# Optimization experiments

Measured on AMD Instinct MI355X. Metric: run time of the kernel, lower is better.

Reference implementation:

```python
import jax, jax.numpy as jnp
import numpy as np

N = 1024      # num_nodes
U = 64        # num_units
IN_DIM = 2    # input feature dim per node
B = 32        # batch
F = IN_DIM + U  # 66, input_size inside _gconv


def _xavier(k, shape):
    fan_in, fan_out = shape[-2], shape[-1]
    std = (2.0 / (fan_in + fan_out)) ** 0.5
    return jax.random.normal(k, shape, jnp.float32) * std


def setup_inputs() -> dict:
    key = jax.random.key(0)
    ks = jax.random.split(key, 14)
    return {
        "inputs": jax.random.normal(ks[0], (B, N * IN_DIM), jnp.float32),
        "hx": jax.random.normal(ks[1], (B, N * U), jnp.float32),
        "adj": jax.random.uniform(ks[2], (2, N, N), jnp.float32),
        "mask": jax.random.uniform(ks[3], (8, N, N), jnp.float32),
        # gate gconv params (output_size = 2U). Note: torch LayerParams caches by
        # shape, so weights_s/weights_i/weights_bp are ONE shared weight, ditto atts/atti.
        "W_ru": _xavier(ks[4], (F, 2 * U)),
        "Watt_ru": _xavier(ks[5], (N, 2 * U, 2 * U)),
        "Watt1_ru": _xavier(ks[6], (N, 2 * U, 1)),
        "Wout_ru": _xavier(ks[7], (6 * U, 2 * U)),
        "b_ru": jnp.ones((2 * U,), jnp.float32),   # bias_start=1.0
        # candidate gconv params (output_size = U)
        "W_c": _xavier(ks[8], (F, U)),
        "Watt_c": _xavier(ks[9], (N, U, U)),
        "Watt1_c": _xavier(ks[10], (N, U, 1)),
        "Wout_c": _xavier(ks[11], (3 * U, U)),
        "b_c": jnp.zeros((U,), jnp.float32),
    }


def _gconv(inputs, state, adj, mask, W, Watt, Watt1, Wout, b):
    Bs = inputs.shape[0]
    x = jnp.concatenate([inputs.reshape(Bs, N, -1), state.reshape(Bs, N, -1)], axis=2)  # [B,N,F]
    Ff = x.shape[2]
    x0 = x.transpose(1, 2, 0).reshape(N, Ff * Bs)  # [N, F*B]
    a0, a1 = adj[0], adj[1]
    # supports in the exact order of the torch loop:
    # adj0, mask0..3*adj0, mask4..7*adj1, adj1  -> 10 matrices
    mats = jnp.concatenate(
        [a0[None], mask[:4] * a0[None], mask[4:] * a1[None], a1[None]], axis=0
    )  # [10,N,N]
    xk = jnp.einsum('mij,jf->mif', mats, x0)  # [10,N,F*B]
    x_all = jnp.concatenate([x0[None], xk], axis=0).reshape(11, N, Ff, Bs)
    x_bp = x_all[0].transpose(2, 0, 1)        # [B,N,F]
    x_i = x_all[1:6].transpose(3, 1, 0, 2)    # [B,N,5,F]
    x_s = x_all[6:].transpose(3, 1, 0, 2)     # [B,N,5,F]
    x_i_p = x_i @ W        # [B,N,5,O] (shared weight, see LayerParams shape cache)
    x_s_p = x_s @ W        # [B,N,5,O]
    x_bp_p = x_bp @ W      # [B,N,O]

    def attend(xp):
        h = jax.nn.relu(jnp.einsum('bnko,noq->bnkq', xp, Watt))     # per-node weights
        s = jnp.einsum('bnkq,nqo->bnko', h, Watt1)[..., 0]          # [B,N,5]
        a = jax.nn.softmax(s, axis=-1)                              # over 5 supports
        return jnp.einsum('bnk,bnko->bno', a, xp)                   # [B,N,O]

    xi = attend(x_i_p)
    xs = attend(x_s_p)
    out = jnp.concatenate([xi, xs, x_bp_p], axis=-1) @ Wout + b     # [B,N,O]
    return out.reshape(Bs, -1)


def reference(inputs, hx, adj, mask, W_ru, Watt_ru, Watt1_ru, Wout_ru, b_ru,
              W_c, Watt_c, Watt1_c, Wout_c, b_c):
    value = jax.nn.sigmoid(_gconv(inputs, hx, adj, mask, W_ru, Watt_ru, Watt1_ru, Wout_ru, b_ru))
    value = value.reshape(-1, N, 2 * U)
    r = value[..., :U].reshape(-1, N * U)
    u = value[..., U:].reshape(-1, N * U)
    c = jnp.tanh(_gconv(inputs, r * hx, adj, mask, W_c, Watt_c, Watt1_c, Wout_c, b_c))
    return u * hx + (1.0 - u) * c
```

## Files before the change

### kernel.cpp

```cpp
#include <hip/hip_runtime.h>
#include <hip/hip_fp16.h>
#include <cstdint>
#include <cstddef>

#define NN 1024
#define BB 32

typedef _Float16 f16x8 __attribute__((ext_vector_type(8)));
typedef _Float16 f16x4 __attribute__((ext_vector_type(4)));
typedef float f32x4 __attribute__((ext_vector_type(4)));
typedef float f32x16 __attribute__((ext_vector_type(16)));

__device__ __forceinline__ void load_lds16(const void* g, void* l) {
  __builtin_amdgcn_global_load_lds(
      (const __attribute__((address_space(1))) void*)g,
      (__attribute__((address_space(3))) void*)l, 16, 0, 0);
}

__global__ __launch_bounds__(256) void k_build_amats(
    const float* __restrict__ adj, const float* __restrict__ mask,
    _Float16* __restrict__ A) {
  int q = blockIdx.x * 256 + threadIdx.x;
  int i = q >> 8;
  int j0 = (q & 255) << 2;
  size_t off = (size_t)i * 1024 + j0;
  float4 a0 = *(const float4*)(adj + off);
  float4 a1 = *(const float4*)(adj + (1u << 20) + off);
  f16x4 r;
  r[0] = a0.x; r[1] = a0.y; r[2] = a0.z; r[3] = a0.w;
  *(f16x4*)(A + off) = r;
  r[0] = a1.x; r[1] = a1.y; r[2] = a1.z; r[3] = a1.w;
  *(f16x4*)(A + (size_t)9 * 1048576 + off) = r;
#pragma unroll
  for (int l = 0; l < 8; ++l) {
    float4 mk = *(const float4*)(mask + (size_t)l * 1048576 + off);
    float4 base = (l < 4) ? a0 : a1;
    r[0] = mk.x * base.x; r[1] = mk.y * base.y;
    r[2] = mk.z * base.z; r[3] = mk.w * base.w;
    *(f16x4*)(A + (size_t)(l + 1) * 1048576 + off) = r;
  }
}

__global__ __launch_bounds__(256) void k_prep_wout(
    const float* __restrict__ Wru, const float* __restrict__ Wc,
    _Float16* __restrict__ WThru, _Float16* __restrict__ WTlru,
    _Float16* __restrict__ WThc, _Float16* __restrict__ WTlc) {
  int id = blockIdx.x * 256 + threadIdx.x;
  if (id < 128 * 384) {
    int o = id & 127, k = id >> 7;
    float w = Wru[k * 128 + o];
    _Float16 h = (_Float16)w;
    WThru[o * 384 + k] = h;
    WTlru[o * 384 + k] = (_Float16)(w - (float)h);
  } else {
    int id2 = id - 128 * 384;
    if (id2 < 64 * 192) {
      int o = id2 & 63, k = id2 >> 6;
      float w = Wc[k * 64 + o];
      _Float16 h = (_Float16)w;
      WThc[o * 192 + k] = h;
      WTlc[o * 192 + k] = (_Float16)(w - (float)h);
    }
  }
}

__global__ __launch_bounds__(256) void k_build_x0p(
    const float* __restrict__ inp, const float* __restrict__ state,
    _Float16* __restrict__ X0P) {
  const int b = blockIdx.x;
  const int j0 = blockIdx.y * 64;
  const int tid = threadIdx.x;
  for (int p = tid; p < 4096; p += 256) {
    int jj = p >> 6, f = p & 63;
    X0P[((size_t)(b * 1024 + j0 + jj)) * 96 + 2 + f] =
        (_Float16)state[(size_t)b * 65536 + (j0 + jj) * 64 + f];
  }
  if (tid < 128) {
    int jj = tid >> 1, f = tid & 1;
    X0P[((size_t)(b * 1024 + j0 + jj)) * 96 + f] =
        (_Float16)inp[(size_t)b * 2048 + (j0 + jj) * 2 + f];
    X0P[((size_t)(b * 1024 + j0 + 32 + jj)) * 96 + f] =
        (_Float16)inp[(size_t)b * 2048 + (j0 + 32 + jj) * 2 + f];
  }
  for (int p = tid; p < 64 * 32; p += 256) {
    int jj = p >> 5, f = 66 + (p & 31);
    if (f < 96)
      X0P[((size_t)(b * 1024 + j0 + jj)) * 96 + f] = (_Float16)0.f;
  }
}

template <int O>
__global__ __launch_bounds__(256, 2) void k_proj0_mfma(
    const _Float16* __restrict__ X0P, const float* __restrict__ W,
    _Float16* __restrict__ XP0, _Float16* __restrict__ XP0T) {
  constexpr int WR = O / 64;
  constexpr int WC = 4 / WR;
  constexpr int TN = WC * 64;
  constexpr int NPT = TN / 64;
  __shared__ _Float16 ldsB[2][TN * 32];
  const int tid = threadIdx.x;
  const int c0 = blockIdx.x * TN;
  const int b = c0 >> 10;
  const int l = tid & 63;
  const int w = tid >> 6;
  const int wr = w / WC, wc = w % WC;

  f16x8 af[4][3];
#pragma unroll
  for (int i = 0; i < 4; ++i) {
    int o = wr * 64 + i * 16 + (l & 15);
#pragma unroll
    for (int ks = 0; ks < 3; ++ks) {
#pragma unroll
      for (int e = 0; e < 8; ++e) {
        int f = ks * 32 + (l >> 4) * 8 + e;
        af[i][ks][e] = (f < 66) ? (_Float16)W[f * O + o] : (_Float16)0.f;
      }
    }
  }

  int tt[NPT], rr[NPT], qq[NPT];
#pragma unroll
  for (int u = 0; u < NPT; ++u) {
    tt[u] = u * 256 + tid;
    rr[u] = tt[u] >> 2;
    qq[u] = (tt[u] & 3) ^ (rr[u] & 3);
  }

  const int ps = ((l >> 4) ^ (l & 3)) * 8;
  int offB[4];
#pragma unroll
  for (int j = 0; j < 4; ++j)
    offB[j] = (wc * 64 + j * 16 + (l & 15)) * 32 + ps;

  f32x4 acc[4][4];
#pragma unroll
  for (int i = 0; i < 4; ++i)
#pragma unroll
    for (int j = 0; j < 4; ++j) acc[i][j] = (f32x4){0.f, 0.f, 0.f, 0.f};

#pragma unroll
  for (int u = 0; u < NPT; ++u)
    load_lds16(X0P + (size_t)(c0 + rr[u]) * 96 + qq[u] * 8,
               &ldsB[0][0] + tt[u] * 8);

  int buf = 0;
  for (int kt = 0; kt < 3; ++kt) {
    __syncthreads();
    if (kt + 1 < 3) {
#pragma unroll
      for (int u = 0; u < NPT; ++u)
        load_lds16(X0P + (size_t)(c0 + rr[u]) * 96 + (kt + 1) * 32 + qq[u] * 8,
                   &ldsB[buf ^ 1][0] + tt[u] * 8);
    }
    f16x8 bf[4];
#pragma unroll
    for (int j = 0; j < 4; ++j) bf[j] = *(const f16x8*)(&ldsB[buf][offB[j]]);
#pragma unroll
    for (int i = 0; i < 4; ++i)
#pragma unroll
      for (int j = 0; j < 4; ++j)
        acc[i][j] = __builtin_amdgcn_mfma_f32_16x16x32_f16(af[i][kt], bf[j],
                                                           acc[i][j], 0, 0, 0);
    buf ^= 1;
  }

#pragma unroll
  for (int i = 0; i < 4; ++i) {
    int ob = wr * 64 + i * 16 + (l >> 4) * 4;
#pragma unroll
    for (int j = 0; j < 4; ++j) {
      int jn = (c0 & 1023) + wc * 64 + j * 16 + (l & 15);
      f16x4 hv;
#pragma unroll
      for (int r = 0; r < 4; ++r) {
        hv[r] = (_Float16)acc[i][j][r];
        XP0T[((size_t)b * O + ob + r) * 1024 + jn] = hv[r];
      }
      *(f16x4*)(XP0 + ((size_t)jn * 32 + b) * O + ob) = hv;
    }
  }
}

template <int CN>
__global__ __launch_bounds__(256, 2) void k_supports2_mfma(
    const _Float16* __restrict__ A, const _Float16* __restrict__ BT,
    _Float16* __restrict__ XPD) {
  __shared__ _Float16 ldsA[2][4096];
  __shared__ _Float16 ldsB[2][4096];
  const int tid = threadIdx.x;
  constexpr int GX = CN / 128;
  const int flat = blockIdx.x + GX * blockIdx.y;
  constexpr int NWG = GX * 80;
  constexpr int CPX = NWG / 8;
  const int swz = (flat & 7) * CPX + (flat >> 3);
  const int bn = swz % GX;
  const int bm = swz / GX;
  const int l = tid & 63;
  const int w = tid >> 6;
  const int wr = w >> 1, wc = w & 1;

  const int t0 = tid, t1 = 256 + tid;
  const int r0 = t0 >> 2, q0 = (t0 & 3) ^ (r0 & 3);
  const int r1 = t1 >> 2, q1 = (t1 & 3) ^ (r1 & 3);
  const _Float16* gA0 = A + ((size_t)(bm * 128 + r0)) * 1024 + q0 * 8;
  const _Float16* gA1 = A + ((size_t)(bm * 128 + r1)) * 1024 + q1 * 8;
  const _Float16* gB0 = BT + ((size_t)(bn * 128 + r0)) * 1024 + q0 * 8;
  const _Float16* gB1 = BT + ((size_t)(bn * 128 + r1)) * 1024 + q1 * 8;

  int offA[2][2], offB[2][2];
#pragma unroll
  for (int fi = 0; fi < 2; ++fi)
#pragma unroll
    for (int ks = 0; ks < 2; ++ks) {
      int slot = ((ks * 2 + (l >> 5)) ^ (l & 3)) * 8;
      offA[fi][ks] = (wr * 64 + fi * 32 + (l & 31)) * 32 + slot;
      offB[fi][ks] = (wc * 64 + fi * 32 + (l & 31)) * 32 + slot;
    }

  f32x16 acc[2][2];
#pragma unroll
  for (int i = 0; i < 2; ++i)
#pragma unroll
    for (int j = 0; j < 2; ++j)
#pragma unroll
      for (int e = 0; e < 16; ++e) acc[i][j][e] = 0.f;

  load_lds16(gA0, &ldsA[0][0] + t0 * 8);
  load_lds16(gA1, &ldsA[0][0] + t1 * 8);
  load_lds16(gB0, &ldsB[0][0] + t0 * 8);
  load_lds16(gB1, &ldsB[0][0] + t1 * 8);

  int buf = 0;
  for (int kt = 0; kt < 32; ++kt) {
    __syncthreads();
    if (kt + 1 < 32) {
      int k0 = (kt + 1) * 32;
      load_lds16(gA0 + k0, &ldsA[buf ^ 1][0] + t0 * 8);
      load_lds16(gA1 + k0, &ldsA[buf ^ 1][0] + t1 * 8);
      load_lds16(gB0 + k0, &ldsB[buf ^ 1][0] + t0 * 8);
      load_lds16(gB1 + k0, &ldsB[buf ^ 1][0] + t1 * 8);
    }
    f16x8 af[2][2], bf[2][2];
#pragma unroll
    for (int fi = 0; fi < 2; ++fi)
#pragma unroll
      for (int ks = 0; ks < 2; ++ks) {
        af[fi][ks] = *(const f16x8*)(&ldsA[buf][offA[fi][ks]]);
        bf[fi][ks] = *(const f16x8*)(&ldsB[buf][offB[fi][ks]]);
      }
#pragma unroll
    for (int fi = 0; fi < 2; ++fi)
#pragma unroll
      for (int fj = 0; fj < 2; ++fj)
#pragma unroll
        for (int ks = 0; ks < 2; ++ks)
          acc[fi][fj] = __builtin_amdgcn_mfma_f32_32x32x16_f16(
              af[fi][ks], bf[fj][ks], acc[fi][fj], 0, 0, 0);
    buf ^= 1;
  }

#pragma unroll
  for (int fi = 0; fi < 2; ++fi)
#pragma unroll
    for (int fj = 0; fj < 2; ++fj) {
      int colg = bn * 128 + wc * 64 + fj * 32 + (l & 31);
      int Rb = bm * 128 + wr * 64 + fi * 32 + 4 * (l >> 5);
#pragma unroll
      for (int e = 0; e < 16; ++e) {
        int R = Rb + (e & 3) + 8 * (e >> 2);
        XPD[(size_t)R * CN + colg] = (_Float16)acc[fi][fj][e];
      }
    }
}

template <int O>
__global__ __launch_bounds__(256) void k_attend_mfma(
    const __half* __restrict__ XPD, const float* __restrict__ Watt,
    const float* __restrict__ Watt1, _Float16* __restrict__ CAT2h,
    _Float16* __restrict__ CAT2l) {
  constexpr int MTW = O / 64;
  constexpr int KS = O / 32;
  constexpr int SLOTS = O / 8;
  constexpr int SWZ = SLOTS - 1;
  constexpr int OH = O / 2;
  const int n = blockIdx.x;
  const int tid = threadIdx.x;
  const int l = tid & 63;
  const int w = tid >> 6;

  __shared__ _Float16 xpL[160 * O];
  __shared__ float sPartL[4][160];
  __shared__ float aL[32][5];

  const int qbase = w * (O / 4);
  f16x8 afr[MTW][KS];
#pragma unroll
  for (int mt = 0; mt < MTW; ++mt) {
    const int q = qbase + mt * 16 + (l & 15);
#pragma unroll
    for (int ks = 0; ks < KS; ++ks) {
#pragma unroll
      for (int e = 0; e < 8; ++e) {
        int o = ks * 32 + (l >> 4) * 8 + e;
        afr[mt][ks][e] = (_Float16)Watt[((size_t)n * O + o) * O + q];
      }
    }
  }
  float wt1[MTW][4];
#pragma unroll
  for (int mt = 0; mt < MTW; ++mt)
#pragma unroll
    for (int r = 0; r < 4; ++r)
      wt1[mt][r] = Watt1[(size_t)n * O + qbase + mt * 16 + (l >> 4) * 4 + r];

  for (int g = 0; g < 2; ++g) {
    if (g) __syncthreads();
    {
      const uint32_t* xsrc = reinterpret_cast<const uint32_t*>(XPD);
      uint32_t* xdst = reinterpret_cast<uint32_t*>(xpL);
      for (int p = tid; p < 160 * OH; p += 256) {
        int row = p / OH;
        int oh = p - row * OH;
        int slot = oh >> 2;
        int phys = slot ^ (row & SWZ);
        int si = row >> 5, b = row & 31;
        size_t gi = ((size_t)(g * 5 + si) * 1024 + n) * (size_t)(16 * O) +
                    b * OH + oh;
        xdst[row * OH + phys * 4 + (oh & 3)] = xsrc[gi];
      }
    }
    __syncthreads();

    for (int nt = 0; nt < 10; ++nt) {
      f32x4 acc[MTW];
#pragma unroll
      for (int mt = 0; mt < MTW; ++mt) acc[mt] = (f32x4){0.f, 0.f, 0.f, 0.f};
      const int row = nt * 16 + (l & 15);
#pragma unroll
      for (int ks = 0; ks < KS; ++ks) {
        int phys = (ks * 4 + (l >> 4)) ^ (row & SWZ);
        f16x8 bf = *(const f16x8*)(&xpL[row * O + phys * 8]);
#pragma unroll
        for (int mt = 0; mt < MTW; ++mt)
          acc[mt] = __builtin_amdgcn_mfma_f32_16x16x32_f16(afr[mt][ks], bf,
                                                           acc[mt], 0, 0, 0);
      }
      float sp = 0.f;
#pragma unroll
      for (int mt = 0; mt < MTW; ++mt)
#pragma unroll
        for (int r = 0; r < 4; ++r)
          sp += fmaxf(acc[mt][r], 0.f) * wt1[mt][r];
      sp += __shfl_xor(sp, 16);
      sp += __shfl_xor(sp, 32);
      if (l < 16) sPartL[w][nt * 16 + l] = sp;
    }
    __syncthreads();

    if (tid < 32) {
      const int b = tid;
      float sv[5];
#pragma unroll
      for (int k = 0; k < 5; ++k) {
        int row = k * 32 + b;
        sv[k] = sPartL[0][row] + sPartL[1][row] + sPartL[2][row] +
                sPartL[3][row];
      }
      float mx = sv[0];
#pragma unroll
      for (int k = 1; k < 5; ++k) mx = fmaxf(mx, sv[k]);
      float e[5], sum = 0.f;
#pragma unroll
      for (int k = 0; k < 5; ++k) {
        e[k] = expf(sv[k] - mx);
        sum += e[k];
      }
      float inv = 1.f / sum;
#pragma unroll
      for (int k = 0; k < 5; ++k) aL[b][k] = e[k] * inv;
    }
    __syncthreads();

    for (int it = 0; it < SLOTS * 32 / 256; ++it) {
      int idx = it * 256 + tid;
      int b = idx & 31;
      int sc = idx >> 5;
      float o8[8] = {0.f, 0.f, 0.f, 0.f, 0.f, 0.f, 0.f, 0.f};
#pragma unroll
      for (int si = 0; si < 5; ++si) {
        int row = si * 32 + b;
        int phys = sc ^ (row & SWZ);
        f16x8 xv = *(const f16x8*)(&xpL[row * O + phys * 8]);
        float a = aL[b][si];
#pragma unroll
        for (int j = 0; j < 8; ++j) o8[j] += a * (float)xv[j];
      }
      f16x8 hv, lv;
#pragma unroll
      for (int j = 0; j < 8; ++j) {
        hv[j] = (_Float16)o8[j];
        lv[j] = (_Float16)(o8[j] - (float)hv[j]);
      }
      size_t doff = ((size_t)n * 32 + b) * (2 * O) + g * O + sc * 8;
      *reinterpret_cast<f16x8*>(CAT2h + doff) = hv;
      *reinterpret_cast<f16x8*>(CAT2l + doff) = lv;
    }
  }
}

__global__ __launch_bounds__(256, 2) void k_wout_ru_mfma(
    const _Float16* __restrict__ CAT2h, const _Float16* __restrict__ CAT2l,
    const _Float16* __restrict__ XP0, const _Float16* __restrict__ WTh,
    const _Float16* __restrict__ WTl, const float* __restrict__ bias,
    const float* __restrict__ hx, float* __restrict__ RHX,
    float* __restrict__ UBUF) {
  constexpr int KTOT = 384, KC = 8, KT = 12;
  __shared__ _Float16 ldsAh[2][4096];
  __shared__ _Float16 ldsAl[2][4096];
  __shared__ _Float16 ldsBh[2][4096];
  __shared__ _Float16 ldsBl[2][4096];
  const int tid = threadIdx.x;
  const int blk = blockIdx.x;
  const int l = tid & 63;
  const int w = tid >> 6;
  const int wr = w >> 1, wc = w & 1;

  const int t0 = tid, t1 = 256 + tid;
  const int r0 = t0 >> 2, q0 = (t0 & 3) ^ (r0 & 3);
  const int r1 = t1 >> 2, q1 = (t1 & 3) ^ (r1 & 3);
  const size_t R0 = (size_t)blk * 128 + r0, R1 = (size_t)blk * 128 + r1;
  const _Float16* pA0ch = CAT2h + R0 * 256 + q0 * 8;
  const _Float16* pA1ch = CAT2h + R1 * 256 + q1 * 8;
  const _Float16* pA0cl = CAT2l + R0 * 256 + q0 * 8;
  const _Float16* pA1cl = CAT2l + R1 * 256 + q1 * 8;
  const _Float16* pA0x = XP0 + R0 * 128 + q0 * 8;
  const _Float16* pA1x = XP0 + R1 * 128 + q1 * 8;
  const _Float16* pB0h = WTh + (size_t)r0 * KTOT + q0 * 8;
  const _Float16* pB1h = WTh + (size_t)r1 * KTOT + q1 * 8;
  const _Float16* pB0l = WTl + (size_t)r0 * KTOT + q0 * 8;
  const _Float16* pB1l = WTl + (size_t)r1 * KTOT + q1 * 8;

  const int ps = ((l >> 4) ^ (l & 3)) * 8;
  int offA[4], offB[4];
#pragma unroll
  for (int i = 0; i < 4; ++i) {
    offA[i] = (wr * 64 + i * 16 + (l & 15)) * 32 + ps;
    offB[i] = (wc * 64 + i * 16 + (l & 15)) * 32 + ps;
  }

  f32x4 acc[4][4];
#pragma unroll
  for (int i = 0; i < 4; ++i)
#pragma unroll
    for (int j = 0; j < 4; ++j) acc[i][j] = (f32x4){0.f, 0.f, 0.f, 0.f};

  load_lds16(pA0ch, &ldsAh[0][0] + t0 * 8);
  load_lds16(pA1ch, &ldsAh[0][0] + t1 * 8);
  load_lds16(pA0cl, &ldsAl[0][0] + t0 * 8);
  load_lds16(pA1cl, &ldsAl[0][0] + t1 * 8);
  load_lds16(pB0h, &ldsBh[0][0] + t0 * 8);
  load_lds16(pB1h, &ldsBh[0][0] + t1 * 8);
  load_lds16(pB0l, &ldsBl[0][0] + t0 * 8);
  load_lds16(pB1l, &ldsBl[0][0] + t1 * 8);

  int buf = 0;
  for (int kt = 0; kt < KT; ++kt) {
    __syncthreads();
    if (kt + 1 < KT) {
      int k1 = kt + 1;
      const _Float16* a0 =
          (k1 < KC) ? pA0ch + k1 * 32 : pA0x + (k1 - KC) * 32;
      const _Float16* a1 =
          (k1 < KC) ? pA1ch + k1 * 32 : pA1x + (k1 - KC) * 32;
      load_lds16(a0, &ldsAh[buf ^ 1][0] + t0 * 8);
      load_lds16(a1, &ldsAh[buf ^ 1][0] + t1 * 8);
      if (k1 < KC) {
        load_lds16(pA0cl + k1 * 32, &ldsAl[buf ^ 1][0] + t0 * 8);
        load_lds16(pA1cl + k1 * 32, &ldsAl[buf ^ 1][0] + t1 * 8);
      }
      load_lds16(pB0h + k1 * 32, &ldsBh[buf ^ 1][0] + t0 * 8);
      load_lds16(pB1h + k1 * 32, &ldsBh[buf ^ 1][0] + t1 * 8);
      load_lds16(pB0l + k1 * 32, &ldsBl[buf ^ 1][0] + t0 * 8);
      load_lds16(pB1l + k1 * 32, &ldsBl[buf ^ 1][0] + t1 * 8);
    }
    f16x8 ah[4], bh[4], bl[4];
#pragma unroll
    for (int i = 0; i < 4; ++i) ah[i] = *(const f16x8*)(&ldsAh[buf][offA[i]]);
#pragma unroll
    for (int i = 0; i < 4; ++i) bh[i] = *(const f16x8*)(&ldsBh[buf][offB[i]]);
#pragma unroll
    for (int i = 0; i < 4; ++i) bl[i] = *(const f16x8*)(&ldsBl[buf][offB[i]]);
#pragma unroll
    for (int i = 0; i < 4; ++i)
#pragma unroll
      for (int j = 0; j < 4; ++j) {
        acc[i][j] = __builtin_amdgcn_mfma_f32_16x16x32_f16(ah[i], bh[j],
                                                           acc[i][j], 0, 0, 0);
        acc[i][j] = __builtin_amdgcn_mfma_f32_16x16x32_f16(ah[i], bl[j],
                                                           acc[i][j], 0, 0, 0);
      }
    if (kt < KC) {
      f16x8 al[4];
#pragma unroll
      for (int i = 0; i < 4; ++i)
        al[i] = *(const f16x8*)(&ldsAl[buf][offA[i]]);
#pragma unroll
      for (int i = 0; i < 4; ++i)
#pragma unroll
        for (int j = 0; j < 4; ++j)
          acc[i][j] = __builtin_amdgcn_mfma_f32_16x16x32_f16(al[i], bh[j],
                                                             acc[i][j], 0, 0, 0);
    }
    buf ^= 1;
  }

#pragma unroll
  for (int i = 0; i < 4; ++i) {
    int R = blk * 128 + wr * 64 + i * 16 + (l >> 4) * 4;
#pragma unroll
    for (int j = 0; j < 4; ++j) {
      int o = wc * 64 + j * 16 + (l & 15);
      float bv = bias[o];
#pragma unroll
      for (int rr = 0; rr < 4; ++rr) {
        int Rr = R + rr;
        int n = Rr >> 5, b = Rr & 31;
        size_t base = ((size_t)b * NN + n) * 64;
        float val = 1.f / (1.f + expf(-(acc[i][j][rr] + bv)));
        if (o < 64)
          RHX[base + o] = val * hx[base + o];
        else
          UBUF[base + (o - 64)] = val;
      }
    }
  }
}

__global__ __launch_bounds__(256, 2) void k_wout_c_mfma(
    const _Float16* __restrict__ CAT2h, const _Float16* __restrict__ XP0,
    const _Float16* __restrict__ WTh, const float* __restrict__ bias,
    const float* __restrict__ UBUF, const float* __restrict__ hx,
    float* __restrict__ out) {
  constexpr int KTOT = 192, KC = 4, KT = 6;
  __shared__ _Float16 ldsAh[2][4096];
  __shared__ _Float16 ldsBh[2][2048];
  const int tid = threadIdx.x;
  const int blk = blockIdx.x;
  const int l = tid & 63;
  const int w = tid >> 6;

  const int t0 = tid, t1 = 256 + tid;
  const int r0 = t0 >> 2, q0 = (t0 & 3) ^ (r0 & 3);
  const int r1 = t1 >> 2, q1 = (t1 & 3) ^ (r1 & 3);
  const size_t R0 = (size_t)blk * 128 + r0, R1 = (size_t)blk * 128 + r1;
  const _Float16* pA0ch = CAT2h + R0 * 128 + q0 * 8;
  const _Float16* pA1ch = CAT2h + R1 * 128 + q1 * 8;
  const _Float16* pA0x = XP0 + R0 * 64 + q0 * 8;
  const _Float16* pA1x = XP0 + R1 * 64 + q1 * 8;
  const int rb = tid >> 2, qb = (tid & 3) ^ (rb & 3);
  const _Float16* pBh = WTh + (size_t)rb * KTOT + qb * 8;

  const int ps = ((l >> 4) ^ (l & 3)) * 8;
  int offA[2], offB[4];
#pragma unroll
  for (int i = 0; i < 2; ++i)
    offA[i] = (w * 32 + i * 16 + (l & 15)) * 32 + ps;
#pragma unroll
  for (int j = 0; j < 4; ++j) offB[j] = (j * 16 + (l & 15)) * 32 + ps;

  f32x4 acc[2][4];
#pragma unroll
  for (int i = 0; i < 2; ++i)
#pragma unroll
    for (int j = 0; j < 4; ++j) acc[i][j] = (f32x4){0.f, 0.f, 0.f, 0.f};

  load_lds16(pA0ch, &ldsAh[0][0] + t0 * 8);
  load_lds16(pA1ch, &ldsAh[0][0] + t1 * 8);
  load_lds16(pBh, &ldsBh[0][0] + tid * 8);

  int buf = 0;
  for (int kt = 0; kt < KT; ++kt) {
    __syncthreads();
    if (kt + 1 < KT) {
      int k1 = kt + 1;
      const _Float16* a0 =
          (k1 < KC) ? pA0ch + k1 * 32 : pA0x + (k1 - KC) * 32;
      const _Float16* a1 =
          (k1 < KC) ? pA1ch + k1 * 32 : pA1x + (k1 - KC) * 32;
      load_lds16(a0, &ldsAh[buf ^ 1][0] + t0 * 8);
      load_lds16(a1, &ldsAh[buf ^ 1][0] + t1 * 8);
      load_lds16(pBh + k1 * 32, &ldsBh[buf ^ 1][0] + tid * 8);
    }
    f16x8 ah[2], bh[4];
#pragma unroll
    for (int i = 0; i < 2; ++i) ah[i] = *(const f16x8*)(&ldsAh[buf][offA[i]]);
#pragma unroll
    for (int j = 0; j < 4; ++j) bh[j] = *(const f16x8*)(&ldsBh[buf][offB[j]]);
#pragma unroll
    for (int i = 0; i < 2; ++i)
#pragma unroll
      for (int j = 0; j < 4; ++j)
        acc[i][j] = __builtin_amdgcn_mfma_f32_16x16x32_f16(ah[i], bh[j],
                                                           acc[i][j], 0, 0, 0);
    buf ^= 1;
  }

#pragma unroll
  for (int i = 0; i < 2; ++i) {
    int R = blk * 128 + w * 32 + i * 16 + (l >> 4) * 4;
#pragma unroll
    for (int j = 0; j < 4; ++j) {
      int o = j * 16 + (l & 15);
      float bv = bias[o];
#pragma unroll
      for (int rr = 0; rr < 4; ++rr) {
        int Rr = R + rr;
        int n = Rr >> 5, b = Rr & 31;
        size_t idx = ((size_t)b * NN + n) * 64 + o;
        float cval = tanhf(acc[i][j][rr] + bv);
        float u = UBUF[idx];
        out[idx] = u * hx[idx] + (1.f - u) * cval;
      }
    }
  }
}

extern "C" void kernel_launch(void* const* d_in, const int* in_sizes, int n_in,
                              void* d_out, int out_size, void* d_ws,
                              size_t ws_size, hipStream_t stream) {
  const float* inputs   = (const float*)d_in[0];
  const float* hx       = (const float*)d_in[1];
  const float* adj      = (const float*)d_in[2];
  const float* mask     = (const float*)d_in[3];
  const float* W_ru     = (const float*)d_in[4];
  const float* Watt_ru  = (const float*)d_in[5];
  const float* Watt1_ru = (const float*)d_in[6];
  const float* Wout_ru  = (const float*)d_in[7];
  const float* b_ru     = (const float*)d_in[8];
  const float* W_c      = (const float*)d_in[9];
  const float* Watt_c   = (const float*)d_in[10];
  const float* Watt1_c  = (const float*)d_in[11];
  const float* Wout_c   = (const float*)d_in[12];
  const float* b_c      = (const float*)d_in[13];

  char* ws = (char*)d_ws;
  _Float16*  X0P   = (_Float16*)(ws);
  _Float16*  XPD   = (_Float16*)(ws + 6291456);
  _Float16*  XP0   = (_Float16*)(ws + 90177536);
  _Float16*  XP0T  = (_Float16*)(ws + 98566144);
  _Float16*  CAT2h = (_Float16*)(ws + 106954752);
  _Float16*  CAT2l = (_Float16*)(ws + 123731968);
  float*     RHX   = (float*)(ws + 140509184);
  float*     UBUF  = (float*)(ws + 148897792);
  _Float16*  A_all = (_Float16*)(ws + 157286400);
  _Float16*  WThru = (_Float16*)(ws + 178257920);
  _Float16*  WTlru = (_Float16*)(ws + 178356224);
  _Float16*  WThc  = (_Float16*)(ws + 178454528);
  _Float16*  WTlc  = (_Float16*)(ws + 178479104);
  float*     out   = (float*)d_out;

  k_build_amats<<<1024, 256, 0, stream>>>(adj, mask, A_all);
  k_prep_wout<<<240, 256, 0, stream>>>(Wout_ru, Wout_c, WThru, WTlru, WThc,
                                       WTlc);

  k_build_x0p<<<dim3(32, 16), 256, 0, stream>>>(inputs, hx, X0P);
  k_proj0_mfma<128><<<256, 256, 0, stream>>>(X0P, W_ru, XP0, XP0T);
  k_supports2_mfma<4096><<<dim3(32, 80), 256, 0, stream>>>(A_all, XP0T, XPD);
  k_attend_mfma<128><<<1024, 256, 0, stream>>>((const __half*)XPD, Watt_ru,
                                               Watt1_ru, CAT2h, CAT2l);
  k_wout_ru_mfma<<<256, 256, 0, stream>>>(CAT2h, CAT2l, XP0, WThru, WTlru,
                                          b_ru, hx, RHX, UBUF);
  k_build_x0p<<<dim3(32, 16), 256, 0, stream>>>(inputs, RHX, X0P);
  k_proj0_mfma<64><<<128, 256, 0, stream>>>(X0P, W_c, XP0, XP0T);
  k_supports2_mfma<2048><<<dim3(16, 80), 256, 0, stream>>>(A_all, XP0T, XPD);
  k_attend_mfma<64><<<1024, 256, 0, stream>>>((const __half*)XPD, Watt_c,
                                              Watt1_c, CAT2h, CAT2l);
  k_wout_c_mfma<<<256, 256, 0, stream>>>(CAT2h, XP0, WThc, b_c,
                                         UBUF, hx, out);
}
```

Before: 374.6 us.

## Rewrite supports GEMM with 256x128 tiles and triple-buffered LDS pipeline

Replaces the double-buffered 128x128 supports GEMM with a 256x128 tile kernel using a three-stage LDS ring, explicit vmcnt waits, and barriers. Global loads for A and B are interleaved between two MFMA half-phases, with setprio raised around the MFMA blocks. The larger M tile halves the number of workgroups and increases reuse of B per A load. The workgroup swizzle is dropped, and the extra LDS per block (about 72KB) may reduce occupancy.

Measured after the change: 358.5 us. 1.04x faster.

```diff
diff --git a/kernel.cpp b/kernel.cpp
--- a/kernel.cpp
+++ b/kernel.cpp
@@ -183,72 +183,92 @@
 }
 
 template <int CN>
-__global__ __launch_bounds__(256, 2) void k_supports2_mfma(
+__global__ __launch_bounds__(256, 2) void k_supports3_mfma(
     const _Float16* __restrict__ A, const _Float16* __restrict__ BT,
     _Float16* __restrict__ XPD) {
-  __shared__ _Float16 ldsA[2][4096];
-  __shared__ _Float16 ldsB[2][4096];
+  __shared__ _Float16 ldsA[3][8192];
+  __shared__ _Float16 ldsB[3][4096];
   const int tid = threadIdx.x;
-  constexpr int GX = CN / 128;
-  const int flat = blockIdx.x + GX * blockIdx.y;
-  constexpr int NWG = GX * 80;
-  constexpr int CPX = NWG / 8;
-  const int swz = (flat & 7) * CPX + (flat >> 3);
-  const int bn = swz % GX;
-  const int bm = swz / GX;
+  const int bn = blockIdx.x;
+  const int bm = blockIdx.y;
   const int l = tid & 63;
   const int w = tid >> 6;
-  const int wr = w >> 1, wc = w & 1;
-
-  const int t0 = tid, t1 = 256 + tid;
-  const int r0 = t0 >> 2, q0 = (t0 & 3) ^ (r0 & 3);
-  const int r1 = t1 >> 2, q1 = (t1 & 3) ^ (r1 & 3);
-  const _Float16* gA0 = A + ((size_t)(bm * 128 + r0)) * 1024 + q0 * 8;
-  const _Float16* gA1 = A + ((size_t)(bm * 128 + r1)) * 1024 + q1 * 8;
-  const _Float16* gB0 = BT + ((size_t)(bn * 128 + r0)) * 1024 + q0 * 8;
-  const _Float16* gB1 = BT + ((size_t)(bn * 128 + r1)) * 1024 + q1 * 8;
-
-  int offA[2][2], offB[2][2];
-#pragma unroll
-  for (int fi = 0; fi < 2; ++fi)
+  const int wm = w >> 1, wn = w & 1;
+
+  const int r0 = tid >> 2;
+  const int lg = (tid & 3) ^ ((r0 >> 1) & 3);
+  const _Float16* gA = A + ((size_t)(bm * 256 + r0)) * 1024 + lg * 8;
+  const _Float16* gB = BT + ((size_t)(bn * 128 + r0)) * 1024 + lg * 8;
+  _Float16* const dA0 = &ldsA[0][0] + tid * 8;
+  _Float16* const dB0 = &ldsB[0][0] + tid * 8;
+
+#define STAGE_A3(t, s)                                      \
+  {                                                         \
+    const _Float16* g_ = gA + (t) * 32;                     \
+    _Float16* d_ = dA0 + (s) * 8192;                        \
+    load_lds16(g_, d_);                                     \
+    load_lds16(g_ + 64 * 1024, d_ + 2048);                  \
+    load_lds16(g_ + 128 * 1024, d_ + 4096);                 \
+    load_lds16(g_ + 192 * 1024, d_ + 6144);                 \
+  }
+#define STAGE_B3(t, s)                                      \
+  {                                                         \
+    const _Float16* g_ = gB + (t) * 32;                     \
+    _Float16* d_ = dB0 + (s) * 4096;                        \
+    load_lds16(g_, d_);                                     \
+    load_lds16(g_ + 64 * 1024, d_ + 2048);                  \
+  }
+
+  const int lr = l & 31, lh = l >> 5;
+  const int sx = (lr >> 1) & 3;
+  int pk[2];
+  pk[0] = lh ^ sx;
+  pk[1] = (2 + lh) ^ sx;
+  int offA_[4][2], offB_[2][2];
+#pragma unroll
+  for (int fi = 0; fi < 4; ++fi)
+#pragma unroll
+    for (int ks = 0; ks < 2; ++ks)
+      offA_[fi][ks] = (wm * 128 + fi * 32 + lr) * 32 + pk[ks] * 8;
+#pragma unroll
+  for (int fj = 0; fj < 2; ++fj)
+#pragma unroll
+    for (int ks = 0; ks < 2; ++ks)
+      offB_[fj][ks] = (wn * 64 + fj * 32 + lr) * 32 + pk[ks] * 8;
+
+  f32x16 acc[4][2];
+#pragma unroll
+  for (int i = 0; i < 4; ++i)
+#pragma unroll
+    for (int j = 0; j < 2; ++j)
+#pragma unroll
+      for (int e = 0; e < 16; ++e) acc[i][j][e] = 0.f;
+
+  STAGE_A3(0, 0); STAGE_B3(0, 0);
+  STAGE_A3(1, 1); STAGE_B3(1, 1);
+
+  int slot = 0;
+  for (int t = 0; t < 32; ++t) {
+    if (t < 31)
+      asm volatile("s_waitcnt vmcnt(6)" ::: "memory");
+    else
+      asm volatile("s_waitcnt vmcnt(0)" ::: "memory");
+    __builtin_amdgcn_sched_barrier(0);
+    __builtin_amdgcn_s_barrier();
+    __builtin_amdgcn_sched_barrier(0);
+    const int s2 = (slot >= 1) ? slot - 1 : slot + 2;
+    if (t + 2 < 32) STAGE_A3(t + 2, s2);
+    f16x8 bf[2][2], af[2][2];
 #pragma unroll
     for (int ks = 0; ks < 2; ++ks) {
-      int slot = ((ks * 2 + (l >> 5)) ^ (l & 3)) * 8;
-      offA[fi][ks] = (wr * 64 + fi * 32 + (l & 31)) * 32 + slot;
-      offB[fi][ks] = (wc * 64 + fi * 32 + (l & 31)) * 32 + slot;
-    }
-
-  f32x16 acc[2][2];
-#pragma unroll
-  for (int i = 0; i < 2; ++i)
-#pragma unroll
-    for (int j = 0; j < 2; ++j)
-#pragma unroll
-      for (int e = 0; e < 16; ++e) acc[i][j][e] = 0.f;
-
-  load_lds16(gA0, &ldsA[0][0] + t0 * 8);
-  load_lds16(gA1, &ldsA[0][0] + t1 * 8);
-  load_lds16(gB0, &ldsB[0][0] + t0 * 8);
-  load_lds16(gB1, &ldsB[0][0] + t1 * 8);
-
-  int buf = 0;
-  for (int kt = 0; kt < 32; ++kt) {
-    __syncthreads();
-    if (kt + 1 < 32) {
-      int k0 = (kt + 1) * 32;
-      load_lds16(gA0 + k0, &ldsA[buf ^ 1][0] + t0 * 8);
-      load_lds16(gA1 + k0, &ldsA[buf ^ 1][0] + t1 * 8);
-      load_lds16(gB0 + k0, &ldsB[buf ^ 1][0] + t0 * 8);
-      load_lds16(gB1 + k0, &ldsB[buf ^ 1][0] + t1 * 8);
-    }
-    f16x8 af[2][2], bf[2][2];
-#pragma unroll
-    for (int fi = 0; fi < 2; ++fi)
-#pragma unroll
-      for (int ks = 0; ks < 2; ++ks) {
-        af[fi][ks] = *(const f16x8*)(&ldsA[buf][offA[fi][ks]]);
-        bf[fi][ks] = *(const f16x8*)(&ldsB[buf][offB[fi][ks]]);
-      }
+      bf[0][ks] = *(const f16x8*)(&ldsB[slot][offB_[0][ks]]);
+      bf[1][ks] = *(const f16x8*)(&ldsB[slot][offB_[1][ks]]);
+      af[0][ks] = *(const f16x8*)(&ldsA[slot][offA_[0][ks]]);
+      af[1][ks] = *(const f16x8*)(&ldsA[slot][offA_[1][ks]]);
+    }
+    asm volatile("s_waitcnt lgkmcnt(0)" ::: "memory");
+    __builtin_amdgcn_sched_barrier(0);
+    __builtin_amdgcn_s_setprio(1);
 #pragma unroll
     for (int fi = 0; fi < 2; ++fi)
 #pragma unroll
@@ -257,21 +277,44 @@
         for (int ks = 0; ks < 2; ++ks)
           acc[fi][fj] = __builtin_amdgcn_mfma_f32_32x32x16_f16(
               af[fi][ks], bf[fj][ks], acc[fi][fj], 0, 0, 0);
-    buf ^= 1;
-  }
-
-#pragma unroll
-  for (int fi = 0; fi < 2; ++fi)
+    __builtin_amdgcn_s_setprio(0);
+    if (t + 2 < 32) STAGE_B3(t + 2, s2);
+    f16x8 ag[2][2];
+#pragma unroll
+    for (int ks = 0; ks < 2; ++ks) {
+      ag[0][ks] = *(const f16x8*)(&ldsA[slot][offA_[2][ks]]);
+      ag[1][ks] = *(const f16x8*)(&ldsA[slot][offA_[3][ks]]);
+    }
+    asm volatile("s_waitcnt lgkmcnt(0)" ::: "memory");
+    __builtin_amdgcn_sched_barrier(0);
+    __builtin_amdgcn_s_setprio(1);
+#pragma unroll
+    for (int fi = 0; fi < 2; ++fi)
+#pragma unroll
+      for (int fj = 0; fj < 2; ++fj)
+#pragma unroll
+        for (int ks = 0; ks < 2; ++ks)
+          acc[fi + 2][fj] = __builtin_amdgcn_mfma_f32_32x32x16_f16(
+              ag[fi][ks], bf[fj][ks], acc[fi + 2][fj], 0, 0, 0);
+    __builtin_amdgcn_s_setprio(0);
+    slot = (slot == 2) ? 0 : slot + 1;
+  }
+
+#pragma unroll
+  for (int fi = 0; fi < 4; ++fi) {
+    int Rb = bm * 256 + wm * 128 + fi * 32 + 4 * lh;
 #pragma unroll
     for (int fj = 0; fj < 2; ++fj) {
-      int colg = bn * 128 + wc * 64 + fj * 32 + (l & 31);
-      int Rb = bm * 128 + wr * 64 + fi * 32 + 4 * (l >> 5);
+      int col = bn * 128 + wn * 64 + fj * 32 + lr;
 #pragma unroll
       for (int e = 0; e < 16; ++e) {
         int R = Rb + (e & 3) + 8 * (e >> 2);
-        XPD[(size_t)R * CN + colg] = (_Float16)acc[fi][fj][e];
-      }
-    }
+        XPD[(size_t)R * CN + col] = (_Float16)acc[fi][fj][e];
+      }
+    }
+  }
+#undef STAGE_A3
+#undef STAGE_B3
 }
 
 template <int O>
@@ -666,14 +709,14 @@
 
   k_build_x0p<<<dim3(32, 16), 256, 0, stream>>>(inputs, hx, X0P);
   k_proj0_mfma<128><<<256, 256, 0, stream>>>(X0P, W_ru, XP0, XP0T);
-  k_supports2_mfma<4096><<<dim3(32, 80), 256, 0, stream>>>(A_all, XP0T, XPD);
+  k_supports3_mfma<4096><<<dim3(32, 40), 256, 0, stream>>>(A_all, XP0T, XPD);
   k_attend_mfma<128><<<1024, 256, 0, stream>>>((const __half*)XPD, Watt_ru,
                                                Watt1_ru, CAT2h, CAT2l);
   k_wout_ru_mfma<<<256, 256, 0, stream>>>(CAT2h, CAT2l, XP0, WThru, WTlru,
                                           b_ru, hx, RHX, UBUF);
   k_build_x0p<<<dim3(32, 16), 256, 0, stream>>>(inputs, RHX, X0P);
   k_proj0_mfma<64><<<128, 256, 0, stream>>>(X0P, W_c, XP0, XP0T);
-  k_supports2_mfma<2048><<<dim3(16, 80), 256, 0, stream>>>(A_all, XP0T, XPD);
+  k_supports3_mfma<2048><<<dim3(16, 40), 256, 0, stream>>>(A_all, XP0T, XPD);
   k_attend_mfma<64><<<1024, 256, 0, stream>>>((const __half*)XPD, Watt_c,
                                               Watt1_c, CAT2h, CAT2l);
   k_wout_c_mfma<<<256, 256, 0, stream>>>(CAT2h, XP0, WThc, b_c,
```
